# Kernel optimization log

Hardware: AMD Instinct MI355X
Metric: run time of the kernel (lower is better)

Reference implementation:

```python
import jax, jax.numpy as jnp
import numpy as np

N_EMBD = 2048
N_HEAD = 16
N_KV_HEAD = 4
HD = N_EMBD // N_HEAD  # 128
B, T = 1, 4096
EPS = 1e-6


def apply_rope(x, cos, sin):
    # x: [B,T,H,hd]; cos/sin: [T,1,hd//2]
    hd = x.shape[-1] // 2
    x1, x2 = x[..., :hd], x[..., hd:]
    y1 = x1 * cos + x2 * sin
    y2 = x2 * cos - x1 * sin
    return jnp.concatenate((y1, y2), axis=-1).astype(x.dtype)


def rms_norm(x, eps=EPS):
    return x * jax.lax.rsqrt(jnp.mean(jnp.square(x), axis=-1, keepdims=True) + eps)


def setup_inputs() -> dict:
    key = jax.random.key(0)
    ks = jax.random.split(key, 7)
    s = 0.02
    return {
        "x": jax.random.normal(ks[0], (B, T, N_EMBD), dtype=jnp.float32),
        "cos": jax.random.normal(ks[1], (T, 1, HD // 2), dtype=jnp.float32),
        "sin": jax.random.normal(ks[2], (T, 1, HD // 2), dtype=jnp.float32),
        "wq": jax.random.normal(ks[3], (N_EMBD, N_HEAD * HD), dtype=jnp.float32) * s,
        "wk": jax.random.normal(ks[4], (N_EMBD, N_KV_HEAD * HD), dtype=jnp.float32) * s,
        "wv": jax.random.normal(ks[5], (N_EMBD, N_KV_HEAD * HD), dtype=jnp.float32) * s,
        "wo": jax.random.normal(ks[6], (N_EMBD, N_EMBD), dtype=jnp.float32) * s,
    }


def reference(x, cos, sin, wq, wk, wv, wo):
    Bb, Tt, C = x.shape
    q = (x @ wq).reshape(Bb, Tt, N_HEAD, HD)
    k = (x @ wk).reshape(Bb, Tt, N_KV_HEAD, HD)
    v = (x @ wv).reshape(Bb, Tt, N_KV_HEAD, HD)
    q = rms_norm(apply_rope(q, cos, sin))
    k = rms_norm(apply_rope(k, cos, sin))
    g = N_HEAD // N_KV_HEAD
    if g > 1:
        k = jnp.repeat(k, g, axis=2)  # [B,T,H,hd]
        v = jnp.repeat(v, g, axis=2)
    scale = 1.0 / jnp.sqrt(jnp.float32(HD))
    # scores: [B,H,T,S]
    scores = jnp.einsum("bthd,bshd->bhts", q, k) * scale
    causal = jnp.tril(jnp.ones((Tt, Tt), dtype=bool))
    scores = jnp.where(causal, scores, jnp.finfo(scores.dtype).min)
    attn = jax.nn.softmax(scores, axis=-1)
    y = jnp.einsum("bhts,bshd->bthd", attn, v).reshape(Bb, Tt, C)
    return y @ wo
```

## Files before the change

kernel.cpp:

```cpp
#include <hip/hip_runtime.h>

#define T_SEQ 4096
#define C_EMB 2048
#define NH 16
#define NKV 4
#define HD 128

typedef short bf16x8 __attribute__((ext_vector_type(8)));
typedef float f32x4 __attribute__((ext_vector_type(4)));
typedef unsigned short u16x4 __attribute__((ext_vector_type(4)));

__device__ inline unsigned short f2bf(float f) {
    unsigned int u = __float_as_uint(f);
    unsigned int r = (u + 0x7FFFu + ((u >> 16) & 1u)) >> 16;
    return (unsigned short)r;
}

__device__ __forceinline__ void async_cp16(const unsigned short* g, unsigned short* l) {
    __builtin_amdgcn_global_load_lds((const __attribute__((address_space(1))) unsigned int*)g,
                                     (__attribute__((address_space(3))) unsigned int*)l,
                                     16, 0, 0);
}

__global__ __launch_bounds__(256) void cvt_bf16(const float* __restrict__ in,
                                                unsigned short* __restrict__ out, int n) {
    int i = (blockIdx.x * 256 + threadIdx.x) * 4;
    if (i >= n) return;
    float4 f = *(const float4*)(&in[i]);
    u16x4 o;
    o.x = f2bf(f.x); o.y = f2bf(f.y); o.z = f2bf(f.z); o.w = f2bf(f.w);
    *(u16x4*)(&out[i]) = o;
}

__global__ __launch_bounds__(256) void transpose_cvt(const float* __restrict__ in, int ld_in,
                                                     int R, int Cc,
                                                     unsigned short* __restrict__ out, int ld_out) {
    __shared__ float tile[32][33];
    int x = blockIdx.x * 32 + threadIdx.x;
    for (int i = threadIdx.y; i < 32; i += 8) {
        int y = blockIdx.y * 32 + i;
        tile[i][threadIdx.x] = in[(size_t)y * ld_in + x];
    }
    __syncthreads();
    int xo = blockIdx.y * 32 + threadIdx.x;
    for (int i = threadIdx.y; i < 32; i += 8) {
        int yo = blockIdx.x * 32 + i;
        out[(size_t)yo * ld_out + xo] = f2bf(tile[threadIdx.x][i]);
    }
}

__global__ __launch_bounds__(256) void gemm_qkv(const unsigned short* __restrict__ A,
                                                const unsigned short* __restrict__ Bt,
                                                const float* __restrict__ cosb,
                                                const float* __restrict__ sinb,
                                                unsigned short* __restrict__ Qn,
                                                unsigned short* __restrict__ Kn,
                                                float* __restrict__ Vbuf) {
    __shared__ __align__(16) unsigned short As[2][128 * 64];
    __shared__ __align__(16) unsigned short Bs[2][128 * 64];
    const int K = 2048;
    int t = threadIdx.x;
    int w = t >> 6, lane = t & 63;
    int ln = lane & 15, q = lane >> 4;
    int wm = w * 32;
    int m0 = blockIdx.y * 128, n0 = blockIdx.x * 128;

    f32x4 acc[2][8] = {};

#pragma unroll
    for (int s = 0; s < 4; ++s) {
        int L = s * 256 + t;
        int r = L >> 3;
        int c = (L & 7) ^ (r & 7);
        async_cp16(&A[(size_t)(m0 + r) * K + c * 8], &As[0][s * 2048 + w * 512]);
        async_cp16(&Bt[(size_t)(n0 + r) * K + c * 8], &Bs[0][s * 2048 + w * 512]);
    }

    for (int it = 0; it < 32; ++it) {
        __syncthreads();
        if (it < 31) {
            int k0 = (it + 1) * 64;
            int p = (it + 1) & 1;
#pragma unroll
            for (int s = 0; s < 4; ++s) {
                int L = s * 256 + t;
                int r = L >> 3;
                int c = (L & 7) ^ (r & 7);
                async_cp16(&A[(size_t)(m0 + r) * K + k0 + c * 8], &As[p][s * 2048 + w * 512]);
                async_cp16(&Bt[(size_t)(n0 + r) * K + k0 + c * 8], &Bs[p][s * 2048 + w * 512]);
            }
        }
        int p = it & 1;
#pragma unroll
        for (int ks = 0; ks < 2; ++ks) {
            int cs = ((ks * 4 + q) ^ (ln & 7)) * 8;
            bf16x8 af[2], bfr[8];
#pragma unroll
            for (int i = 0; i < 2; ++i) af[i] = *(const bf16x8*)(&As[p][(wm + i * 16 + ln) * 64 + cs]);
#pragma unroll
            for (int j = 0; j < 8; ++j) bfr[j] = *(const bf16x8*)(&Bs[p][(j * 16 + ln) * 64 + cs]);
#pragma unroll
            for (int i = 0; i < 2; ++i)
#pragma unroll
                for (int j = 0; j < 8; ++j)
                    acc[i][j] = __builtin_amdgcn_mfma_f32_16x16x32_bf16(af[i], bfr[j], acc[i][j], 0, 0, 0);
        }
    }

    if (n0 < 2560) {
        bool isQ = (n0 < 2048);
        int h = isQ ? (n0 >> 7) : ((n0 - 2048) >> 7);
#pragma unroll
        for (int i = 0; i < 2; ++i)
#pragma unroll
            for (int r = 0; r < 4; ++r) {
                int row = m0 + wm + i * 16 + q * 4 + r;
                float y1[4], y2[4];
                float ss = 0.0f;
#pragma unroll
                for (int j = 0; j < 4; ++j) {
                    float a = acc[i][j][r];
                    float b = acc[i][j + 4][r];
                    float cc = cosb[row * 64 + j * 16 + ln];
                    float sv = sinb[row * 64 + j * 16 + ln];
                    y1[j] = a * cc + b * sv;
                    y2[j] = b * cc - a * sv;
                    ss += y1[j] * y1[j] + y2[j] * y2[j];
                }
                ss += __shfl_xor(ss, 1);
                ss += __shfl_xor(ss, 2);
                ss += __shfl_xor(ss, 4);
                ss += __shfl_xor(ss, 8);
                float rv = rsqrtf(ss * (1.0f / 128.0f) + 1e-6f);
                if (isQ) {
                    float s = rv * (0.08838834764831845f * 1.4426950408889634f);
                    unsigned short* ob = Qn + (size_t)row * 2048 + h * 128;
#pragma unroll
                    for (int j = 0; j < 4; ++j) {
                        ob[j * 16 + ln] = f2bf(y1[j] * s);
                        ob[64 + j * 16 + ln] = f2bf(y2[j] * s);
                    }
                } else {
                    unsigned short* ob = Kn + (size_t)row * 512 + h * 128;
#pragma unroll
                    for (int j = 0; j < 4; ++j) {
                        ob[j * 16 + ln] = f2bf(y1[j] * rv);
                        ob[64 + j * 16 + ln] = f2bf(y2[j] * rv);
                    }
                }
            }
    } else {
        int v0 = n0 - 2560;
#pragma unroll
        for (int i = 0; i < 2; ++i)
#pragma unroll
            for (int j = 0; j < 8; ++j)
#pragma unroll
                for (int r = 0; r < 4; ++r) {
                    int row = m0 + wm + i * 16 + q * 4 + r;
                    Vbuf[(size_t)row * 512 + v0 + j * 16 + ln] = acc[i][j][r];
                }
    }
}

__global__ __launch_bounds__(256) void gemm_bt_db(const unsigned short* __restrict__ A,
                                                  const unsigned short* __restrict__ Bt,
                                                  float* __restrict__ C, int M, int N, int K) {
    __shared__ __align__(16) unsigned short As[2][128 * 64];
    __shared__ __align__(16) unsigned short Bs[2][128 * 64];
    int t = threadIdx.x;
    int w = t >> 6, lane = t & 63;
    int ln = lane & 15, q = lane >> 4;
    int wm = (w >> 1) * 64, wn = (w & 1) * 64;
    int m0 = blockIdx.y * 128, n0 = blockIdx.x * 128;

    f32x4 acc[4][4] = {};

#pragma unroll
    for (int s = 0; s < 4; ++s) {
        int L = s * 256 + t;
        int r = L >> 3;
        int c = (L & 7) ^ (r & 7);
        async_cp16(&A[(size_t)(m0 + r) * K + c * 8], &As[0][s * 2048 + w * 512]);
        async_cp16(&Bt[(size_t)(n0 + r) * K + c * 8], &Bs[0][s * 2048 + w * 512]);
    }

    int niter = K >> 6;
    for (int it = 0; it < niter; ++it) {
        __syncthreads();
        if (it < niter - 1) {
            int k0 = (it + 1) * 64;
            int p = (it + 1) & 1;
#pragma unroll
            for (int s = 0; s < 4; ++s) {
                int L = s * 256 + t;
                int r = L >> 3;
                int c = (L & 7) ^ (r & 7);
                async_cp16(&A[(size_t)(m0 + r) * K + k0 + c * 8], &As[p][s * 2048 + w * 512]);
                async_cp16(&Bt[(size_t)(n0 + r) * K + k0 + c * 8], &Bs[p][s * 2048 + w * 512]);
            }
        }
        int p = it & 1;
#pragma unroll
        for (int ks = 0; ks < 2; ++ks) {
            int cs = ((ks * 4 + q) ^ (ln & 7)) * 8;
            bf16x8 af[4], bfr[4];
#pragma unroll
            for (int i = 0; i < 4; ++i) af[i] = *(const bf16x8*)(&As[p][(wm + i * 16 + ln) * 64 + cs]);
#pragma unroll
            for (int j = 0; j < 4; ++j) bfr[j] = *(const bf16x8*)(&Bs[p][(wn + j * 16 + ln) * 64 + cs]);
#pragma unroll
            for (int i = 0; i < 4; ++i)
#pragma unroll
                for (int j = 0; j < 4; ++j)
                    acc[i][j] = __builtin_amdgcn_mfma_f32_16x16x32_bf16(af[i], bfr[j], acc[i][j], 0, 0, 0);
        }
    }
#pragma unroll
    for (int i = 0; i < 4; ++i)
#pragma unroll
        for (int j = 0; j < 4; ++j)
#pragma unroll
            for (int r = 0; r < 4; ++r) {
                int row = m0 + wm + i * 16 + q * 4 + r;
                int col = n0 + wn + j * 16 + ln;
                C[(size_t)row * N + col] = acc[i][j][r];
            }
}

__global__ __launch_bounds__(256) void flash_attn(const unsigned short* __restrict__ Qn,
                                                  const unsigned short* __restrict__ Kn,
                                                  const unsigned short* __restrict__ Vt,
                                                  unsigned short* __restrict__ Ao) {
    __shared__ __align__(16) unsigned short Ks[2][64 * 128];
    __shared__ __align__(16) unsigned short Vs[2][128 * 64];
    __shared__ __align__(16) unsigned short Pl[4][16 * 72];

    int pairi = blockIdx.x;
    int h = blockIdx.y;
    int kvh = h >> 2;
    int t = threadIdx.x;
    int w = t >> 6, lane = t & 63;
    int ln = lane & 15, q = lane >> 4;

    int nA = 64 - pairi;
    int bq = 63 - pairi;
    int wq0 = bq * 64 + w * 16;

    bf16x8 qf[4];
    {
        const unsigned short* qb = Qn + (size_t)(wq0 + ln) * 2048 + h * 128;
#pragma unroll
        for (int kc = 0; kc < 4; ++kc) qf[kc] = *(const bf16x8*)(qb + kc * 32 + q * 8);
    }

    f32x4 o[8] = {};
    f32x4 l_p = {0.f, 0.f, 0.f, 0.f};

#pragma unroll
    for (int s = 0; s < 4; ++s) {
        int L = s * 256 + t;
        int key = L >> 4;
        int c = (L & 15) ^ (key & 15);
        async_cp16(Kn + (size_t)key * 512 + kvh * 128 + c * 8, &Ks[0][s * 2048 + w * 512]);
    }
#pragma unroll
    for (int s = 0; s < 4; ++s) {
        int L = s * 256 + t;
        int hd = L >> 3;
        int c = (L & 7) ^ (hd & 7);
        async_cp16(Vt + (size_t)(kvh * 128 + hd) * 4096 + c * 8, &Vs[0][s * 2048 + w * 512]);
    }

    for (int it = 0; it < 65; ++it) {
        __syncthreads();

        int nxt = it + 1;
        if (nxt < 65) {
            int nkt = (nxt < nA) ? nxt * 64 : (nxt - nA) * 64;
            unsigned short* kd = Ks[nxt & 1];
            unsigned short* vd = Vs[nxt & 1];
#pragma unroll
            for (int s = 0; s < 4; ++s) {
                int L = s * 256 + t;
                int key = L >> 4;
                int c = (L & 15) ^ (key & 15);
                async_cp16(Kn + (size_t)(nkt + key) * 512 + kvh * 128 + c * 8,
                           kd + s * 2048 + w * 512);
            }
#pragma unroll
            for (int s = 0; s < 4; ++s) {
                int L = s * 256 + t;
                int hd = L >> 3;
                int c = (L & 7) ^ (hd & 7);
                async_cp16(Vt + (size_t)(kvh * 128 + hd) * 4096 + nkt + c * 8,
                           vd + s * 2048 + w * 512);
            }
        }

        if (it == nA) {
#pragma unroll
            for (int r = 0; r < 4; ++r) {
                float lsum = l_p[r];
                lsum += __shfl_xor(lsum, 1);
                lsum += __shfl_xor(lsum, 2);
                lsum += __shfl_xor(lsum, 4);
                lsum += __shfl_xor(lsum, 8);
                float inv = 1.0f / lsum;
                int row = wq0 + q * 4 + r;
                unsigned short* ob = Ao + (size_t)row * 2048 + h * 128;
#pragma unroll
                for (int f = 0; f < 8; ++f) ob[f * 16 + ln] = f2bf(o[f][r] * inv);
            }
            bq = pairi;
            wq0 = bq * 64 + w * 16;
            const unsigned short* qb = Qn + (size_t)(wq0 + ln) * 2048 + h * 128;
#pragma unroll
            for (int kc = 0; kc < 4; ++kc) qf[kc] = *(const bf16x8*)(qb + kc * 32 + q * 8);
#pragma unroll
            for (int f = 0; f < 8; ++f) o[f] = (f32x4){0.f, 0.f, 0.f, 0.f};
            l_p = (f32x4){0.f, 0.f, 0.f, 0.f};
        }

        int kt0 = (it < nA) ? it * 64 : (it - nA) * 64;
        const unsigned short* kb = Ks[it & 1];
        const unsigned short* vb = Vs[it & 1];

        f32x4 sA[4] = {{-16.6f, -16.6f, -16.6f, -16.6f}, {-16.6f, -16.6f, -16.6f, -16.6f},
                       {-16.6f, -16.6f, -16.6f, -16.6f}, {-16.6f, -16.6f, -16.6f, -16.6f}};
#pragma unroll
        for (int jt = 0; jt < 4; ++jt) {
            int key = jt * 16 + ln;
#pragma unroll
            for (int kc = 0; kc < 4; ++kc) {
                int cs = ((kc * 4 + q) ^ ln) * 8;
                bf16x8 kf = *(const bf16x8*)(&kb[key * 128 + cs]);
                sA[jt] = __builtin_amdgcn_mfma_f32_16x16x32_bf16(qf[kc], kf, sA[jt], 0, 0, 0);
            }
        }
        if (kt0 + 63 > wq0) {
#pragma unroll
            for (int jt = 0; jt < 4; ++jt)
#pragma unroll
                for (int r = 0; r < 4; ++r) {
                    int key = kt0 + jt * 16 + ln;
                    int row = wq0 + q * 4 + r;
                    if (key > row) sA[jt][r] = -3e38f;
                }
        }
#pragma unroll
        for (int r = 0; r < 4; ++r) {
            int prow = (q * 4 + r) * 72;
#pragma unroll
            for (int jt = 0; jt < 4; ++jt) {
                float p = __builtin_amdgcn_exp2f(sA[jt][r]);
                Pl[w][prow + jt * 16 + ln] = (unsigned short)(__float_as_uint(p) >> 16);
                l_p[r] += p;
            }
        }

#pragma unroll
        for (int ks = 0; ks < 2; ++ks) {
            bf16x8 pa = *(const bf16x8*)(&Pl[w][ln * 72 + ks * 32 + q * 8]);
            int cs = ((ks * 4 + q) ^ (ln & 7)) * 8;
#pragma unroll
            for (int f = 0; f < 8; ++f) {
                bf16x8 vf = *(const bf16x8*)(&vb[(f * 16 + ln) * 64 + cs]);
                o[f] = __builtin_amdgcn_mfma_f32_16x16x32_bf16(pa, vf, o[f], 0, 0, 0);
            }
        }
    }
#pragma unroll
    for (int r = 0; r < 4; ++r) {
        float lsum = l_p[r];
        lsum += __shfl_xor(lsum, 1);
        lsum += __shfl_xor(lsum, 2);
        lsum += __shfl_xor(lsum, 4);
        lsum += __shfl_xor(lsum, 8);
        float inv = 1.0f / lsum;
        int row = wq0 + q * 4 + r;
        unsigned short* ob = Ao + (size_t)row * 2048 + h * 128;
#pragma unroll
        for (int f = 0; f < 8; ++f) ob[f * 16 + ln] = f2bf(o[f][r] * inv);
    }
}

extern "C" void kernel_launch(void* const* d_in, const int* in_sizes, int n_in,
                              void* d_out, int out_size, void* d_ws, size_t ws_size,
                              hipStream_t stream) {
    const float* x    = (const float*)d_in[0];
    const float* cosb = (const float*)d_in[1];
    const float* sinb = (const float*)d_in[2];
    const float* wq   = (const float*)d_in[3];
    const float* wk   = (const float*)d_in[4];
    const float* wv   = (const float*)d_in[5];
    const float* wo   = (const float*)d_in[6];
    float* out = (float*)d_out;

    char* ws = (char*)d_ws;
    float* Vbuf = (float*)ws;
    unsigned short* xb    = (unsigned short*)(ws + (size_t)4096 * 3072 * 4);
    unsigned short* wqkvT = xb    + (size_t)4096 * 2048;
    unsigned short* woT   = wqkvT + (size_t)3072 * 2048;
    unsigned short* Qn    = woT   + (size_t)2048 * 2048;
    unsigned short* Kn    = Qn    + (size_t)4096 * 2048;
    unsigned short* Vt    = Kn    + (size_t)4096 * 512;
    unsigned short* Ao    = Vt    + (size_t)512 * 4096;

    cvt_bf16<<<(4096 * 2048 / 4 + 255) / 256, 256, 0, stream>>>(x, xb, 4096 * 2048);
    transpose_cvt<<<dim3(64, 64), dim3(32, 8), 0, stream>>>(wq, 2048, 2048, 2048, wqkvT, 2048);
    transpose_cvt<<<dim3(16, 64), dim3(32, 8), 0, stream>>>(wk, 512, 2048, 512, wqkvT + (size_t)2048 * 2048, 2048);
    transpose_cvt<<<dim3(16, 64), dim3(32, 8), 0, stream>>>(wv, 512, 2048, 512, wqkvT + (size_t)2560 * 2048, 2048);
    transpose_cvt<<<dim3(64, 64), dim3(32, 8), 0, stream>>>(wo, 2048, 2048, 2048, woT, 2048);
    gemm_qkv<<<dim3(24, 32), 256, 0, stream>>>(xb, wqkvT, cosb, sinb, Qn, Kn, Vbuf);
    transpose_cvt<<<dim3(16, 128), dim3(32, 8), 0, stream>>>(Vbuf, 512, 4096, 512, Vt, 4096);
    flash_attn<<<dim3(32, 16), 256, 0, stream>>>(Qn, Kn, Vt, Ao);
    gemm_bt_db<<<dim3(16, 32), 256, 0, stream>>>(Ao, woT, out, 4096, 2048, 2048);
}
```

Measured before the change: 373.0 us.

## Fuse V transpose into QKV GEMM, merge weight transposes, shrink K-tile

Four weight transpose launches are merged into one z-indexed kernel. The V path of the QKV GEMM now writes a bf16 transposed V directly through shared memory, which removes the fp32 V buffer and a separate transpose launch. Both GEMMs change their K tile from 64 to 32 with an adjusted XOR swizzle and add an occupancy hint of 4 blocks per SIMD. In exchange, each GEMM runs twice as many K iterations and barriers, and some transpose blocks exit early and do nothing.

```diff
diff --git a/kernel.cpp b/kernel.cpp
--- a/kernel.cpp
+++ b/kernel.cpp
@@ -32,10 +32,23 @@
     *(u16x4*)(&out[i]) = o;
 }
 
-__global__ __launch_bounds__(256) void transpose_cvt(const float* __restrict__ in, int ld_in,
-                                                     int R, int Cc,
-                                                     unsigned short* __restrict__ out, int ld_out) {
+__global__ __launch_bounds__(256) void transpose_all(const float* __restrict__ wq,
+                                                     const float* __restrict__ wk,
+                                                     const float* __restrict__ wv,
+                                                     const float* __restrict__ wo,
+                                                     unsigned short* __restrict__ wqkvT,
+                                                     unsigned short* __restrict__ woT) {
     __shared__ float tile[32][33];
+    int z = blockIdx.z;
+    const float* in;
+    unsigned short* out;
+    int ld_in;
+    if (z == 0)      { in = wq; out = wqkvT;                         ld_in = 2048; }
+    else if (z == 1) { in = wk; out = wqkvT + (size_t)2048 * 2048;   ld_in = 512;  }
+    else if (z == 2) { in = wv; out = wqkvT + (size_t)2560 * 2048;   ld_in = 512;  }
+    else             { in = wo; out = woT;                           ld_in = 2048; }
+    if ((z == 1 || z == 2) && blockIdx.x >= 16) return;
+
     int x = blockIdx.x * 32 + threadIdx.x;
     for (int i = threadIdx.y; i < 32; i += 8) {
         int y = blockIdx.y * 32 + i;
@@ -45,19 +58,19 @@
     int xo = blockIdx.y * 32 + threadIdx.x;
     for (int i = threadIdx.y; i < 32; i += 8) {
         int yo = blockIdx.x * 32 + i;
-        out[(size_t)yo * ld_out + xo] = f2bf(tile[threadIdx.x][i]);
-    }
-}
-
-__global__ __launch_bounds__(256) void gemm_qkv(const unsigned short* __restrict__ A,
-                                                const unsigned short* __restrict__ Bt,
-                                                const float* __restrict__ cosb,
-                                                const float* __restrict__ sinb,
-                                                unsigned short* __restrict__ Qn,
-                                                unsigned short* __restrict__ Kn,
-                                                float* __restrict__ Vbuf) {
-    __shared__ __align__(16) unsigned short As[2][128 * 64];
-    __shared__ __align__(16) unsigned short Bs[2][128 * 64];
+        out[(size_t)yo * 2048 + xo] = f2bf(tile[threadIdx.x][i]);
+    }
+}
+
+__global__ __launch_bounds__(256, 4) void gemm_qkv(const unsigned short* __restrict__ A,
+                                                   const unsigned short* __restrict__ Bt,
+                                                   const float* __restrict__ cosb,
+                                                   const float* __restrict__ sinb,
+                                                   unsigned short* __restrict__ Qn,
+                                                   unsigned short* __restrict__ Kn,
+                                                   unsigned short* __restrict__ Vt) {
+    __shared__ __align__(16) unsigned short As[2][128 * 32];
+    __shared__ __align__(16) unsigned short Bs[2][128 * 32];
     const int K = 2048;
     int t = threadIdx.x;
     int w = t >> 6, lane = t & 63;
@@ -68,43 +81,40 @@
     f32x4 acc[2][8] = {};
 
 #pragma unroll
-    for (int s = 0; s < 4; ++s) {
+    for (int s = 0; s < 2; ++s) {
         int L = s * 256 + t;
-        int r = L >> 3;
-        int c = (L & 7) ^ (r & 7);
+        int r = L >> 2;
+        int c = (L & 3) ^ ((L >> 4) & 3);
         async_cp16(&A[(size_t)(m0 + r) * K + c * 8], &As[0][s * 2048 + w * 512]);
         async_cp16(&Bt[(size_t)(n0 + r) * K + c * 8], &Bs[0][s * 2048 + w * 512]);
     }
 
-    for (int it = 0; it < 32; ++it) {
+    for (int it = 0; it < 64; ++it) {
         __syncthreads();
-        if (it < 31) {
-            int k0 = (it + 1) * 64;
+        if (it < 63) {
+            int k0 = (it + 1) * 32;
             int p = (it + 1) & 1;
 #pragma unroll
-            for (int s = 0; s < 4; ++s) {
+            for (int s = 0; s < 2; ++s) {
                 int L = s * 256 + t;
-                int r = L >> 3;
-                int c = (L & 7) ^ (r & 7);
+                int r = L >> 2;
+                int c = (L & 3) ^ ((L >> 4) & 3);
                 async_cp16(&A[(size_t)(m0 + r) * K + k0 + c * 8], &As[p][s * 2048 + w * 512]);
                 async_cp16(&Bt[(size_t)(n0 + r) * K + k0 + c * 8], &Bs[p][s * 2048 + w * 512]);
             }
         }
         int p = it & 1;
-#pragma unroll
-        for (int ks = 0; ks < 2; ++ks) {
-            int cs = ((ks * 4 + q) ^ (ln & 7)) * 8;
-            bf16x8 af[2], bfr[8];
-#pragma unroll
-            for (int i = 0; i < 2; ++i) af[i] = *(const bf16x8*)(&As[p][(wm + i * 16 + ln) * 64 + cs]);
-#pragma unroll
-            for (int j = 0; j < 8; ++j) bfr[j] = *(const bf16x8*)(&Bs[p][(j * 16 + ln) * 64 + cs]);
-#pragma unroll
-            for (int i = 0; i < 2; ++i)
-#pragma unroll
-                for (int j = 0; j < 8; ++j)
-                    acc[i][j] = __builtin_amdgcn_mfma_f32_16x16x32_bf16(af[i], bfr[j], acc[i][j], 0, 0, 0);
-        }
+        int cs = (q ^ ((ln >> 2) & 3)) * 8;
+        bf16x8 af[2], bfr[8];
+#pragma unroll
+        for (int i = 0; i < 2; ++i) af[i] = *(const bf16x8*)(&As[p][(wm + i * 16 + ln) * 32 + cs]);
+#pragma unroll
+        for (int j = 0; j < 8; ++j) bfr[j] = *(const bf16x8*)(&Bs[p][(j * 16 + ln) * 32 + cs]);
+#pragma unroll
+        for (int i = 0; i < 2; ++i)
+#pragma unroll
+            for (int j = 0; j < 8; ++j)
+                acc[i][j] = __builtin_amdgcn_mfma_f32_16x16x32_bf16(af[i], bfr[j], acc[i][j], 0, 0, 0);
     }
 
     if (n0 < 2560) {
@@ -151,23 +161,39 @@
             }
     } else {
         int v0 = n0 - 2560;
-#pragma unroll
-        for (int i = 0; i < 2; ++i)
-#pragma unroll
-            for (int j = 0; j < 8; ++j)
-#pragma unroll
-                for (int r = 0; r < 4; ++r) {
-                    int row = m0 + wm + i * 16 + q * 4 + r;
-                    Vbuf[(size_t)row * 512 + v0 + j * 16 + ln] = acc[i][j][r];
+        unsigned short* sm = &As[0][0];
+#pragma unroll
+        for (int half = 0; half < 2; ++half) {
+            __syncthreads();
+#pragma unroll
+            for (int i = 0; i < 2; ++i)
+#pragma unroll
+                for (int jj = 0; jj < 4; ++jj) {
+                    int j = half * 4 + jj;
+                    int cc = jj * 16 + ln;
+                    int rr = wm + i * 16 + q * 4;
+                    u16x4 pk;
+                    pk.x = f2bf(acc[i][j][0]); pk.y = f2bf(acc[i][j][1]);
+                    pk.z = f2bf(acc[i][j][2]); pk.w = f2bf(acc[i][j][3]);
+                    *(u16x4*)(&sm[cc * 136 + rr]) = pk;
                 }
-    }
-}
-
-__global__ __launch_bounds__(256) void gemm_bt_db(const unsigned short* __restrict__ A,
-                                                  const unsigned short* __restrict__ Bt,
-                                                  float* __restrict__ C, int M, int N, int K) {
-    __shared__ __align__(16) unsigned short As[2][128 * 64];
-    __shared__ __align__(16) unsigned short Bs[2][128 * 64];
+            __syncthreads();
+            int vtr = t >> 2, mseg = (t & 3) * 32;
+            unsigned short* dst = Vt + (size_t)(v0 + half * 64 + vtr) * 4096 + m0 + mseg;
+            const unsigned short* src = &sm[vtr * 136 + mseg];
+            *(int4*)(dst)      = *(const int4*)(src);
+            *(int4*)(dst + 8)  = *(const int4*)(src + 8);
+            *(int4*)(dst + 16) = *(const int4*)(src + 16);
+            *(int4*)(dst + 24) = *(const int4*)(src + 24);
+        }
+    }
+}
+
+__global__ __launch_bounds__(256, 4) void gemm_bt_db(const unsigned short* __restrict__ A,
+                                                     const unsigned short* __restrict__ Bt,
+                                                     float* __restrict__ C, int M, int N, int K) {
+    __shared__ __align__(16) unsigned short As[2][128 * 32];
+    __shared__ __align__(16) unsigned short Bs[2][128 * 32];
     int t = threadIdx.x;
     int w = t >> 6, lane = t & 63;
     int ln = lane & 15, q = lane >> 4;
@@ -177,44 +203,41 @@
     f32x4 acc[4][4] = {};
 
 #pragma unroll
-    for (int s = 0; s < 4; ++s) {
+    for (int s = 0; s < 2; ++s) {
         int L = s * 256 + t;
-        int r = L >> 3;
-        int c = (L & 7) ^ (r & 7);
+        int r = L >> 2;
+        int c = (L & 3) ^ ((L >> 4) & 3);
         async_cp16(&A[(size_t)(m0 + r) * K + c * 8], &As[0][s * 2048 + w * 512]);
         async_cp16(&Bt[(size_t)(n0 + r) * K + c * 8], &Bs[0][s * 2048 + w * 512]);
     }
 
-    int niter = K >> 6;
+    int niter = K >> 5;
     for (int it = 0; it < niter; ++it) {
         __syncthreads();
         if (it < niter - 1) {
-            int k0 = (it + 1) * 64;
+            int k0 = (it + 1) * 32;
             int p = (it + 1) & 1;
 #pragma unroll
-            for (int s = 0; s < 4; ++s) {
+            for (int s = 0; s < 2; ++s) {
                 int L = s * 256 + t;
-                int r = L >> 3;
-                int c = (L & 7) ^ (r & 7);
+                int r = L >> 2;
+                int c = (L & 3) ^ ((L >> 4) & 3);
                 async_cp16(&A[(size_t)(m0 + r) * K + k0 + c * 8], &As[p][s * 2048 + w * 512]);
                 async_cp16(&Bt[(size_t)(n0 + r) * K + k0 + c * 8], &Bs[p][s * 2048 + w * 512]);
             }
         }
         int p = it & 1;
-#pragma unroll
-        for (int ks = 0; ks < 2; ++ks) {
-            int cs = ((ks * 4 + q) ^ (ln & 7)) * 8;
-            bf16x8 af[4], bfr[4];
-#pragma unroll
-            for (int i = 0; i < 4; ++i) af[i] = *(const bf16x8*)(&As[p][(wm + i * 16 + ln) * 64 + cs]);
-#pragma unroll
-            for (int j = 0; j < 4; ++j) bfr[j] = *(const bf16x8*)(&Bs[p][(wn + j * 16 + ln) * 64 + cs]);
-#pragma unroll
-            for (int i = 0; i < 4; ++i)
-#pragma unroll
-                for (int j = 0; j < 4; ++j)
-                    acc[i][j] = __builtin_amdgcn_mfma_f32_16x16x32_bf16(af[i], bfr[j], acc[i][j], 0, 0, 0);
-        }
+        int cs = (q ^ ((ln >> 2) & 3)) * 8;
+        bf16x8 af[4], bfr[4];
+#pragma unroll
+        for (int i = 0; i < 4; ++i) af[i] = *(const bf16x8*)(&As[p][(wm + i * 16 + ln) * 32 + cs]);
+#pragma unroll
+        for (int j = 0; j < 4; ++j) bfr[j] = *(const bf16x8*)(&Bs[p][(wn + j * 16 + ln) * 32 + cs]);
+#pragma unroll
+        for (int i = 0; i < 4; ++i)
+#pragma unroll
+            for (int j = 0; j < 4; ++j)
+                acc[i][j] = __builtin_amdgcn_mfma_f32_16x16x32_bf16(af[i], bfr[j], acc[i][j], 0, 0, 0);
     }
 #pragma unroll
     for (int i = 0; i < 4; ++i)
@@ -398,8 +421,7 @@
     float* out = (float*)d_out;
 
     char* ws = (char*)d_ws;
-    float* Vbuf = (float*)ws;
-    unsigned short* xb    = (unsigned short*)(ws + (size_t)4096 * 3072 * 4);
+    unsigned short* xb    = (unsigned short*)ws;
     unsigned short* wqkvT = xb    + (size_t)4096 * 2048;
     unsigned short* woT   = wqkvT + (size_t)3072 * 2048;
     unsigned short* Qn    = woT   + (size_t)2048 * 2048;
@@ -408,12 +430,8 @@
     unsigned short* Ao    = Vt    + (size_t)512 * 4096;
 
     cvt_bf16<<<(4096 * 2048 / 4 + 255) / 256, 256, 0, stream>>>(x, xb, 4096 * 2048);
-    transpose_cvt<<<dim3(64, 64), dim3(32, 8), 0, stream>>>(wq, 2048, 2048, 2048, wqkvT, 2048);
-    transpose_cvt<<<dim3(16, 64), dim3(32, 8), 0, stream>>>(wk, 512, 2048, 512, wqkvT + (size_t)2048 * 2048, 2048);
-    transpose_cvt<<<dim3(16, 64), dim3(32, 8), 0, stream>>>(wv, 512, 2048, 512, wqkvT + (size_t)2560 * 2048, 2048);
-    transpose_cvt<<<dim3(64, 64), dim3(32, 8), 0, stream>>>(wo, 2048, 2048, 2048, woT, 2048);
-    gemm_qkv<<<dim3(24, 32), 256, 0, stream>>>(xb, wqkvT, cosb, sinb, Qn, Kn, Vbuf);
-    transpose_cvt<<<dim3(16, 128), dim3(32, 8), 0, stream>>>(Vbuf, 512, 4096, 512, Vt, 4096);
+    transpose_all<<<dim3(64, 64, 4), dim3(32, 8), 0, stream>>>(wq, wk, wv, wo, wqkvT, woT);
+    gemm_qkv<<<dim3(24, 32), 256, 0, stream>>>(xb, wqkvT, cosb, sinb, Qn, Kn, Vt);
     flash_attn<<<dim3(32, 16), 256, 0, stream>>>(Qn, Kn, Vt, Ao);
     gemm_bt_db<<<dim3(16, 32), 256, 0, stream>>>(Ao, woT, out, 4096, 2048, 2048);
 }
```

Result: faster. 363.8 us (-2.5%).
